# Kernel tuning notes

Hardware: AMD Instinct MI355X
Metric: run time of the kernel (lower is better)

The kernel has to match this reference:

```python
import jax, jax.numpy as jnp
import numpy as np

EPS = 0.0001
N, E, DIN, H, DH, C, G = 50000, 800000, 256, 4, 64, 10, 100


def setup_inputs() -> dict:
    key = jax.random.key(0)
    ks = jax.random.split(key, 10)
    x = jax.random.normal(ks[0], (N, DIN), dtype=jnp.float32)
    src = jax.random.randint(ks[1], (E,), 0, N)
    dst = jax.random.randint(ks[2], (E,), 0, N)
    midx = jnp.stack([src, dst]).astype(jnp.int32)
    batch = jnp.sort(jax.random.randint(ks[3], (N,), 0, G)).astype(jnp.int32)
    W_feat = jax.random.normal(ks[4], (DIN, H * DH), dtype=jnp.float32) / np.sqrt(DIN)
    phi = jax.random.normal(ks[5], (H, 2 * DH, 1), dtype=jnp.float32) / np.sqrt(2 * DH)
    W1 = jax.random.normal(ks[6], (H * DH, DH), dtype=jnp.float32) / np.sqrt(H * DH)
    b1 = jnp.zeros((DH,), jnp.float32)
    W2 = jax.random.normal(ks[7], (DH, C), dtype=jnp.float32) / np.sqrt(DH)
    b2 = jnp.zeros((C,), jnp.float32)
    return {"x": x, "midx": midx, "batch": batch, "W_feat": W_feat,
            "phi": phi, "W1": W1, "b1": b1, "W2": W2, "b2": b2}


def reference(x, midx, batch, W_feat, phi, W1, b1, W2, b2):
    src, dst = midx[0], midx[1]
    # per-head node features [N, H, DH]
    h = (x @ W_feat).reshape(-1, H, DH)
    # concat-then-matmul with phi == sum of two half projections (GAT trick)
    phi_s = phi[:, :DH, 0]   # [H, DH]
    phi_d = phi[:, DH:, 0]   # [H, DH]
    a_s = jnp.einsum('nhd,hd->nh', h, phi_s)  # [N, H]
    a_d = jnp.einsum('nhd,hd->nh', h, phi_d)
    w = jax.nn.sigmoid(jax.nn.leaky_relu(a_s[src] + a_d[dst]))  # [E, H]
    msg = (h[dst] * w[:, :, None]).reshape(src.shape[0], H * DH)  # [E, H*DH]
    agg = jax.ops.segment_sum(msg, src, num_segments=x.shape[0])  # scatter_add
    # MLP head (dropout is identity in eval mode)
    z = jax.nn.leaky_relu(agg @ W1 + b1) @ W2 + b2  # [N, C]
    tmp = jnp.exp(z - jnp.max(z, axis=-1, keepdims=True)) + EPS
    preds = tmp / jnp.sum(tmp, axis=-1, keepdims=True)
    # global mean pool over graphs
    sums = jax.ops.segment_sum(preds, batch, num_segments=G)
    cnts = jax.ops.segment_sum(jnp.ones((batch.shape[0],), preds.dtype), batch, num_segments=G)
    yp = sums / cnts[:, None]
    return jnp.log(yp), preds
```

## Files before the change

### kernel.cpp

```cpp
#include <hip/hip_runtime.h>
#include <hip/hip_bf16.h>
#include <cstdint>

#define NN   50000
#define EE   800000
#define DIN_ 256
#define HD_  256
#define DH_  64
#define NH_  4
#define NC_  10
#define NG_  100
#define EPS_ 1e-4f
#define SLOPE_ 0.01f
#define AROW 40
#define CAP_ 48
#define AGGW 5120

typedef unsigned short ushortT;
typedef __attribute__((ext_vector_type(8))) short short8;
typedef __attribute__((ext_vector_type(4))) float f32x4;

__device__ __forceinline__ float leaky(float x) { return x >= 0.f ? x : SLOPE_ * x; }
__device__ __forceinline__ float sigm(float x)  { return 1.f / (1.f + __expf(-x)); }
__device__ __forceinline__ float b2f(ushortT u) { return __uint_as_float(((unsigned)u) << 16); }
__device__ __forceinline__ ushortT f2b(float f) {
    unsigned u = __float_as_uint(f);
    u += 0x7fffu + ((u >> 16) & 1u);
    return (ushortT)(u >> 16);
}

__global__ void setup_kernel(int* cursor,
                             const float* __restrict__ W, ushortT* __restrict__ wt,
                             const float* __restrict__ W1, ushortT* __restrict__ w1t,
                             const int* __restrict__ batch, int* __restrict__ gstart) {
    int i = blockIdx.x * 256 + threadIdx.x;
    if (i < NN) {
        cursor[i] = 0;
        int b = batch[i];
        int bp = (i == 0) ? -1 : batch[i - 1];
        for (int g = bp + 1; g <= b; g++) gstart[g] = i;
        if (i == NN - 1) {
            for (int g = b + 1; g <= NG_; g++) gstart[g] = NN;
        }
    }
    if (i < DIN_ * HD_) {
        int k = i >> 8, n = i & 255;
        wt[n * DIN_ + k] = f2b(W[i]);
    }
    if (i < 256 * 64) {
        int k = i >> 6, o = i & 63;
        w1t[o * 256 + k] = f2b(W1[i]);
    }
}

__global__ __launch_bounds__(256) void gemm_attn(const float* __restrict__ x,
                                                 const ushortT* __restrict__ wt,
                                                 const float* __restrict__ phi,
                                                 ushortT* __restrict__ hbf,
                                                 float* __restrict__ a_s,
                                                 float* __restrict__ a_d) {
    __shared__ ushortT A_lds[128 * AROW];
    __shared__ ushortT B_lds[128 * AROW];
    const int tid  = threadIdx.x;
    const int wave = tid >> 6, lane = tid & 63;
    const int wm = wave >> 1, wn = wave & 1;
    const int row0 = blockIdx.x * 128;
    const int col0 = blockIdx.y * 128;
    const int q = lane >> 4, l16 = lane & 15;

    f32x4 acc[4][4];
#pragma unroll
    for (int i = 0; i < 4; i++)
#pragma unroll
        for (int j = 0; j < 4; j++) acc[i][j] = (f32x4){0.f, 0.f, 0.f, 0.f};

    const int lm  = tid >> 1;
    const int lko = (tid & 1) * 16;

    for (int k0 = 0; k0 < DIN_; k0 += 32) {
        __syncthreads();
        {
            int gr = row0 + lm;
            float4 a0 = make_float4(0.f,0.f,0.f,0.f), a1 = a0, a2 = a0, a3 = a0;
            if (gr < NN) {
                const float4* xp = (const float4*)(x + (size_t)gr * DIN_ + k0 + lko);
                a0 = xp[0]; a1 = xp[1]; a2 = xp[2]; a3 = xp[3];
            }
            ushortT* ap = &A_lds[lm * AROW + lko];
            *(ushort4*)(ap + 0)  = make_ushort4(f2b(a0.x), f2b(a0.y), f2b(a0.z), f2b(a0.w));
            *(ushort4*)(ap + 4)  = make_ushort4(f2b(a1.x), f2b(a1.y), f2b(a1.z), f2b(a1.w));
            *(ushort4*)(ap + 8)  = make_ushort4(f2b(a2.x), f2b(a2.y), f2b(a2.z), f2b(a2.w));
            *(ushort4*)(ap + 12) = make_ushort4(f2b(a3.x), f2b(a3.y), f2b(a3.z), f2b(a3.w));
        }
        {
            const uint4* wp = (const uint4*)(wt + (size_t)(col0 + lm) * DIN_ + k0 + lko);
            uint4 b0 = wp[0], b1 = wp[1];
            *(uint4*)&B_lds[lm * AROW + lko + 0] = b0;
            *(uint4*)&B_lds[lm * AROW + lko + 8] = b1;
        }
        __syncthreads();

        short8 af[4], bf[4];
#pragma unroll
        for (int mi = 0; mi < 4; mi++)
            af[mi] = *(const short8*)&A_lds[(wm * 64 + mi * 16 + l16) * AROW + q * 8];
#pragma unroll
        for (int ni = 0; ni < 4; ni++)
            bf[ni] = *(const short8*)&B_lds[(wn * 64 + ni * 16 + l16) * AROW + q * 8];
#pragma unroll
        for (int mi = 0; mi < 4; mi++)
#pragma unroll
            for (int ni = 0; ni < 4; ni++)
                acc[mi][ni] = __builtin_amdgcn_mfma_f32_16x16x32_bf16(af[mi], bf[ni], acc[mi][ni], 0, 0, 0);
    }

#pragma unroll
    for (int mi = 0; mi < 4; mi++) {
        int rbase = row0 + wm * 64 + mi * 16 + q * 4;
#pragma unroll
        for (int ni = 0; ni < 4; ni++) {
            int c = col0 + wn * 64 + ni * 16 + l16;
#pragma unroll
            for (int r = 0; r < 4; r++) {
                int gr = rbase + r;
                if (gr < NN) hbf[(size_t)gr * HD_ + c] = f2b(acc[mi][ni][r]);
            }
        }
    }

    int head = blockIdx.y * 2 + wn;
    float phs[4], phd[4];
#pragma unroll
    for (int ni = 0; ni < 4; ni++) {
        phs[ni] = phi[head * 128 + ni * 16 + l16];
        phd[ni] = phi[head * 128 + 64 + ni * 16 + l16];
    }
#pragma unroll
    for (int mi = 0; mi < 4; mi++) {
#pragma unroll
        for (int r = 0; r < 4; r++) {
            float ps = acc[mi][0][r] * phs[0] + acc[mi][1][r] * phs[1]
                     + acc[mi][2][r] * phs[2] + acc[mi][3][r] * phs[3];
            float pd = acc[mi][0][r] * phd[0] + acc[mi][1][r] * phd[1]
                     + acc[mi][2][r] * phd[2] + acc[mi][3][r] * phd[3];
#pragma unroll
            for (int o = 1; o < 16; o <<= 1) {
                ps += __shfl_xor(ps, o);
                pd += __shfl_xor(pd, o);
            }
            if (l16 == 0) {
                int gr = row0 + wm * 64 + mi * 16 + q * 4 + r;
                if (gr < NN) {
                    a_s[gr * 4 + head] = ps;
                    a_d[gr * 4 + head] = pd;
                }
            }
        }
    }
}

__global__ void fill_edges(const int* __restrict__ src, const int* __restrict__ dstA,
                           int* __restrict__ cursor,
                           const float* __restrict__ a_s, const float* __restrict__ a_d,
                           uint4* __restrict__ edges) {
    int e = blockIdx.x * 256 + threadIdx.x;
    if (e >= EE) return;
    int s = src[e], d = dstA[e];
    int slot = atomicAdd(&cursor[s], 1);
    if (slot >= CAP_) return;
    float4 as4 = *(const float4*)(a_s + (size_t)s * 4);
    float4 ad4 = *(const float4*)(a_d + (size_t)d * 4);
    unsigned w01 = (unsigned)f2b(sigm(leaky(as4.x + ad4.x)))
                 | ((unsigned)f2b(sigm(leaky(as4.y + ad4.y))) << 16);
    unsigned w23 = (unsigned)f2b(sigm(leaky(as4.z + ad4.z)))
                 | ((unsigned)f2b(sigm(leaky(as4.w + ad4.w))) << 16);
    edges[(size_t)s * CAP_ + slot] = make_uint4((unsigned)d, w01, w23, 0u);
}

__global__ __launch_bounds__(256) void agg_kernel(const ushortT* __restrict__ hbf,
                                                  const int* __restrict__ cursor,
                                                  const uint4* __restrict__ edges,
                                                  ushortT* __restrict__ aggB) {
    int wid = blockIdx.x * 4 + (threadIdx.x >> 6);
    int lane = threadIdx.x & 63;
    int hsel = lane >> 4;
    int wsh = (hsel & 1) * 16;
    const ushortT* hbase = hbf + (size_t)lane * 4;

    for (int n = wid; n < NN; n += AGGW) {
        int cnt = cursor[n];
        if (cnt > CAP_) cnt = CAP_;
        int e0 = n * CAP_, e1 = e0 + cnt;
        float4 acc = make_float4(0.f, 0.f, 0.f, 0.f);

        int i = e0;
        while (i + 8 <= e1) {
            uint4 ee[8]; ushort4 hh[8]; float ww[8];
#pragma unroll
            for (int j = 0; j < 8; j++) ee[j] = edges[i + j];
#pragma unroll
            for (int j = 0; j < 8; j++) {
                unsigned pair = (hsel & 2) ? ee[j].z : ee[j].y;
                ww[j] = b2f((ushortT)((pair >> wsh) & 0xffffu));
                hh[j] = *(const ushort4*)(hbase + (size_t)ee[j].x * HD_);
            }
#pragma unroll
            for (int j = 0; j < 8; j++) {
                acc.x += b2f(hh[j].x) * ww[j];
                acc.y += b2f(hh[j].y) * ww[j];
                acc.z += b2f(hh[j].z) * ww[j];
                acc.w += b2f(hh[j].w) * ww[j];
            }
            i += 8;
        }
        while (i + 4 <= e1) {
            uint4 ee[4]; ushort4 hh[4]; float ww[4];
#pragma unroll
            for (int j = 0; j < 4; j++) ee[j] = edges[i + j];
#pragma unroll
            for (int j = 0; j < 4; j++) {
                unsigned pair = (hsel & 2) ? ee[j].z : ee[j].y;
                ww[j] = b2f((ushortT)((pair >> wsh) & 0xffffu));
                hh[j] = *(const ushort4*)(hbase + (size_t)ee[j].x * HD_);
            }
#pragma unroll
            for (int j = 0; j < 4; j++) {
                acc.x += b2f(hh[j].x) * ww[j];
                acc.y += b2f(hh[j].y) * ww[j];
                acc.z += b2f(hh[j].z) * ww[j];
                acc.w += b2f(hh[j].w) * ww[j];
            }
            i += 4;
        }
        for (; i < e1; i++) {
            uint4 e = edges[i];
            unsigned pair = (hsel & 2) ? e.z : e.y;
            float s = b2f((ushortT)((pair >> wsh) & 0xffffu));
            ushort4 hv = *(const ushort4*)(hbase + (size_t)e.x * HD_);
            acc.x += b2f(hv.x) * s; acc.y += b2f(hv.y) * s;
            acc.z += b2f(hv.z) * s; acc.w += b2f(hv.w) * s;
        }
        ushort4 o4 = make_ushort4(f2b(acc.x), f2b(acc.y), f2b(acc.z), f2b(acc.w));
        *(ushort4*)(aggB + (size_t)n * HD_ + lane * 4) = o4;
    }
}

__global__ __launch_bounds__(256) void mlp_kernel(const ushortT* __restrict__ aggB,
                                                  const ushortT* __restrict__ w1t,
                                                  const float* __restrict__ b1,
                                                  const float* __restrict__ W2,
                                                  const float* __restrict__ b2,
                                                  float* __restrict__ out) {
    __shared__ float z1t[64][65];
    const int tid = threadIdx.x;
    const int wave = tid >> 6, lane = tid & 63;
    const int q = lane >> 4, l16 = lane & 15;
    const int n0 = blockIdx.x * 64;
    const int nodeRow = n0 + wave * 16 + l16;

    f32x4 acc[4];
#pragma unroll
    for (int ni = 0; ni < 4; ni++) acc[ni] = (f32x4){0.f, 0.f, 0.f, 0.f};

    const ushortT* arow = aggB + (size_t)nodeRow * HD_ + q * 8;
#pragma unroll
    for (int k0 = 0; k0 < 256; k0 += 32) {
        short8 af = *(const short8*)(arow + k0);
#pragma unroll
        for (int ni = 0; ni < 4; ni++) {
            short8 bf = *(const short8*)(w1t + (size_t)(ni * 16 + l16) * 256 + k0 + q * 8);
            acc[ni] = __builtin_amdgcn_mfma_f32_16x16x32_bf16(af, bf, acc[ni], 0, 0, 0);
        }
    }
#pragma unroll
    for (int ni = 0; ni < 4; ni++) {
        int o = ni * 16 + l16;
        float bb = b1[o];
#pragma unroll
        for (int r = 0; r < 4; r++)
            z1t[o][wave * 16 + q * 4 + r] = leaky(acc[ni][r] + bb);
    }
    __syncthreads();

    if (tid < 64) {
        int n = n0 + tid;
        if (n < NN) {
            float zc[NC_];
#pragma unroll
            for (int c = 0; c < NC_; c++) zc[c] = b2[c];
            for (int k = 0; k < 64; k++) {
                float zv = z1t[k][tid];
#pragma unroll
                for (int c = 0; c < NC_; c++) zc[c] += zv * W2[k * NC_ + c];
            }
            float m = zc[0];
#pragma unroll
            for (int c = 1; c < NC_; c++) m = fmaxf(m, zc[c]);
            float ssum = 0.f;
#pragma unroll
            for (int c = 0; c < NC_; c++) { zc[c] = __expf(zc[c] - m) + EPS_; ssum += zc[c]; }
            float inv = 1.f / ssum;
#pragma unroll
            for (int c = 0; c < NC_; c++) out[1000 + (size_t)n * NC_ + c] = zc[c] * inv;
        }
    }
}

__global__ __launch_bounds__(256) void group_mean(const float* __restrict__ preds,
                                                  const int* __restrict__ gstart,
                                                  float* __restrict__ out) {
    __shared__ float red[16][16];
    int g = blockIdx.x;
    int t = threadIdx.x;
    int c = t & 15, chunk = t >> 4;
    int gs = gstart[g], ge = gstart[g + 1];
    float s = 0.f;
    if (c < NC_) {
        for (int n = gs + chunk; n < ge; n += 16) s += preds[(size_t)n * NC_ + c];
    }
    red[chunk][c] = s;
    __syncthreads();
    if (t < NC_) {
        float tot = 0.f;
#pragma unroll
        for (int j = 0; j < 16; j++) tot += red[j][t];
        out[g * NC_ + t] = __logf(tot / (float)(ge - gs));
    }
}

extern "C" void kernel_launch(void* const* d_in, const int* in_sizes, int n_in,
                              void* d_out, int out_size, void* d_ws, size_t ws_size,
                              hipStream_t stream) {
    const float* x      = (const float*)d_in[0];
    const int*   midx   = (const int*)d_in[1];
    const int*   batch  = (const int*)d_in[2];
    const float* W_feat = (const float*)d_in[3];
    const float* phi    = (const float*)d_in[4];
    const float* W1     = (const float*)d_in[5];
    const float* b1     = (const float*)d_in[6];
    const float* W2     = (const float*)d_in[7];
    const float* b2     = (const float*)d_in[8];
    const int* src = midx;
    const int* dst = midx + EE;
    float* out = (float*)d_out;

    char* p = (char*)d_ws;
    auto alloc = [&](size_t bytes) { void* r = (void*)p; p += (bytes + 255) & ~(size_t)255; return r; };
    ushortT* hbf      = (ushortT*)alloc((size_t)NN * HD_ * 2);
    ushortT* aggB     = (ushortT*)alloc((size_t)NN * HD_ * 2);
    uint4*   edges    = (uint4*)alloc((size_t)NN * CAP_ * 16);
    ushortT* wt       = (ushortT*)alloc((size_t)DIN_ * HD_ * 2);
    ushortT* w1t      = (ushortT*)alloc((size_t)64 * 256 * 2);
    float*   a_s      = (float*)alloc((size_t)NN * 4 * 4);
    float*   a_d      = (float*)alloc((size_t)NN * 4 * 4);
    int*     cursor   = (int*)alloc((size_t)NN * 4);
    int*     gstart   = (int*)alloc((size_t)(NG_ + 1) * 4);

    setup_kernel<<<256, 256, 0, stream>>>(cursor, W_feat, wt, W1, w1t, batch, gstart);
    gemm_attn<<<dim3((NN + 127) / 128, 2), 256, 0, stream>>>(x, wt, phi, hbf, a_s, a_d);
    fill_edges<<<(EE + 255) / 256, 256, 0, stream>>>(src, dst, cursor, a_s, a_d, edges);
    agg_kernel<<<AGGW / 4, 256, 0, stream>>>(hbf, cursor, edges, aggB);
    mlp_kernel<<<(NN + 63) / 64, 256, 0, stream>>>(aggB, w1t, b1, W2, b2, out);
    group_mean<<<NG_, 256, 0, stream>>>(out + 1000, gstart, out);
}
```

Before: 272.7 us.

## Compute all heads per GEMM block and move edge weights into aggregation

The GEMM now computes all 256 output columns (every head) per 128-row block, so each block reads its x tile once instead of twice. Edge attention weights are no longer precomputed in fill_edges. That kernel now stores only the destination index (4 bytes instead of a 16-byte record), and the aggregation kernel computes sigmoid(leaky(a_s+a_d)) on the fly. Aggregation launches one wave per node instead of a persistent grid-stride loop. The trade-offs are higher register pressure in the GEMM, which adds launch_bounds(256,1) and doubles the accumulators, and extra a_d gathers plus transcendental work inside the aggregation.

```diff
diff --git a/kernel.cpp b/kernel.cpp
--- a/kernel.cpp
+++ b/kernel.cpp
@@ -14,7 +14,6 @@
 #define SLOPE_ 0.01f
 #define AROW 40
 #define CAP_ 48
-#define AGGW 5120
 
 typedef unsigned short ushortT;
 typedef __attribute__((ext_vector_type(8))) short short8;
@@ -53,24 +52,22 @@
     }
 }
 
-__global__ __launch_bounds__(256) void gemm_attn(const float* __restrict__ x,
-                                                 const ushortT* __restrict__ wt,
-                                                 const float* __restrict__ phi,
-                                                 ushortT* __restrict__ hbf,
-                                                 float* __restrict__ a_s,
-                                                 float* __restrict__ a_d) {
+__global__ __launch_bounds__(256, 1) void gemm_attn(const float* __restrict__ x,
+                                                    const ushortT* __restrict__ wt,
+                                                    const float* __restrict__ phi,
+                                                    ushortT* __restrict__ hbf,
+                                                    float* __restrict__ a_s,
+                                                    float* __restrict__ a_d) {
     __shared__ ushortT A_lds[128 * AROW];
-    __shared__ ushortT B_lds[128 * AROW];
+    __shared__ ushortT B_lds[256 * AROW];
     const int tid  = threadIdx.x;
     const int wave = tid >> 6, lane = tid & 63;
-    const int wm = wave >> 1, wn = wave & 1;
     const int row0 = blockIdx.x * 128;
-    const int col0 = blockIdx.y * 128;
     const int q = lane >> 4, l16 = lane & 15;
 
-    f32x4 acc[4][4];
-#pragma unroll
-    for (int i = 0; i < 4; i++)
+    f32x4 acc[8][4];
+#pragma unroll
+    for (int i = 0; i < 8; i++)
 #pragma unroll
         for (int j = 0; j < 4; j++) acc[i][j] = (f32x4){0.f, 0.f, 0.f, 0.f};
 
@@ -93,33 +90,34 @@
             *(ushort4*)(ap + 12) = make_ushort4(f2b(a3.x), f2b(a3.y), f2b(a3.z), f2b(a3.w));
         }
         {
-            const uint4* wp = (const uint4*)(wt + (size_t)(col0 + lm) * DIN_ + k0 + lko);
-            uint4 b0 = wp[0], b1 = wp[1];
-            *(uint4*)&B_lds[lm * AROW + lko + 0] = b0;
-            *(uint4*)&B_lds[lm * AROW + lko + 8] = b1;
+            const uint4* wp = (const uint4*)(wt + (size_t)tid * DIN_ + k0);
+            uint4 b0 = wp[0], b1 = wp[1], b2 = wp[2], b3 = wp[3];
+            *(uint4*)&B_lds[tid * AROW + 0]  = b0;
+            *(uint4*)&B_lds[tid * AROW + 8]  = b1;
+            *(uint4*)&B_lds[tid * AROW + 16] = b2;
+            *(uint4*)&B_lds[tid * AROW + 24] = b3;
         }
         __syncthreads();
 
-        short8 af[4], bf[4];
-#pragma unroll
-        for (int mi = 0; mi < 4; mi++)
-            af[mi] = *(const short8*)&A_lds[(wm * 64 + mi * 16 + l16) * AROW + q * 8];
+        short8 bf[4];
 #pragma unroll
         for (int ni = 0; ni < 4; ni++)
-            bf[ni] = *(const short8*)&B_lds[(wn * 64 + ni * 16 + l16) * AROW + q * 8];
-#pragma unroll
-        for (int mi = 0; mi < 4; mi++)
+            bf[ni] = *(const short8*)&B_lds[(wave * 64 + ni * 16 + l16) * AROW + q * 8];
+#pragma unroll
+        for (int mi = 0; mi < 8; mi++) {
+            short8 af = *(const short8*)&A_lds[(mi * 16 + l16) * AROW + q * 8];
 #pragma unroll
             for (int ni = 0; ni < 4; ni++)
-                acc[mi][ni] = __builtin_amdgcn_mfma_f32_16x16x32_bf16(af[mi], bf[ni], acc[mi][ni], 0, 0, 0);
-    }
-
-#pragma unroll
-    for (int mi = 0; mi < 4; mi++) {
-        int rbase = row0 + wm * 64 + mi * 16 + q * 4;
+                acc[mi][ni] = __builtin_amdgcn_mfma_f32_16x16x32_bf16(af, bf[ni], acc[mi][ni], 0, 0, 0);
+        }
+    }
+
+#pragma unroll
+    for (int mi = 0; mi < 8; mi++) {
+        int rbase = row0 + mi * 16 + q * 4;
 #pragma unroll
         for (int ni = 0; ni < 4; ni++) {
-            int c = col0 + wn * 64 + ni * 16 + l16;
+            int c = wave * 64 + ni * 16 + l16;
 #pragma unroll
             for (int r = 0; r < 4; r++) {
                 int gr = rbase + r;
@@ -128,15 +126,14 @@
         }
     }
 
-    int head = blockIdx.y * 2 + wn;
     float phs[4], phd[4];
 #pragma unroll
     for (int ni = 0; ni < 4; ni++) {
-        phs[ni] = phi[head * 128 + ni * 16 + l16];
-        phd[ni] = phi[head * 128 + 64 + ni * 16 + l16];
-    }
-#pragma unroll
-    for (int mi = 0; mi < 4; mi++) {
+        phs[ni] = phi[wave * 128 + ni * 16 + l16];
+        phd[ni] = phi[wave * 128 + 64 + ni * 16 + l16];
+    }
+#pragma unroll
+    for (int mi = 0; mi < 8; mi++) {
 #pragma unroll
         for (int r = 0; r < 4; r++) {
             float ps = acc[mi][0][r] * phs[0] + acc[mi][1][r] * phs[1]
@@ -149,10 +146,10 @@
                 pd += __shfl_xor(pd, o);
             }
             if (l16 == 0) {
-                int gr = row0 + wm * 64 + mi * 16 + q * 4 + r;
+                int gr = row0 + mi * 16 + q * 4 + r;
                 if (gr < NN) {
-                    a_s[gr * 4 + head] = ps;
-                    a_d[gr * 4 + head] = pd;
+                    a_s[gr * 4 + wave] = ps;
+                    a_d[gr * 4 + wave] = pd;
                 }
             }
         }
@@ -160,89 +157,79 @@
 }
 
 __global__ void fill_edges(const int* __restrict__ src, const int* __restrict__ dstA,
-                           int* __restrict__ cursor,
-                           const float* __restrict__ a_s, const float* __restrict__ a_d,
-                           uint4* __restrict__ edges) {
+                           int* __restrict__ cursor, int* __restrict__ edge_dst) {
     int e = blockIdx.x * 256 + threadIdx.x;
     if (e >= EE) return;
-    int s = src[e], d = dstA[e];
+    int s = src[e];
     int slot = atomicAdd(&cursor[s], 1);
     if (slot >= CAP_) return;
-    float4 as4 = *(const float4*)(a_s + (size_t)s * 4);
-    float4 ad4 = *(const float4*)(a_d + (size_t)d * 4);
-    unsigned w01 = (unsigned)f2b(sigm(leaky(as4.x + ad4.x)))
-                 | ((unsigned)f2b(sigm(leaky(as4.y + ad4.y))) << 16);
-    unsigned w23 = (unsigned)f2b(sigm(leaky(as4.z + ad4.z)))
-                 | ((unsigned)f2b(sigm(leaky(as4.w + ad4.w))) << 16);
-    edges[(size_t)s * CAP_ + slot] = make_uint4((unsigned)d, w01, w23, 0u);
+    edge_dst[s * CAP_ + slot] = dstA[e];
 }
 
 __global__ __launch_bounds__(256) void agg_kernel(const ushortT* __restrict__ hbf,
                                                   const int* __restrict__ cursor,
-                                                  const uint4* __restrict__ edges,
+                                                  const int* __restrict__ edge_dst,
+                                                  const float* __restrict__ a_s,
+                                                  const float* __restrict__ a_d,
                                                   ushortT* __restrict__ aggB) {
-    int wid = blockIdx.x * 4 + (threadIdx.x >> 6);
-    int lane = threadIdx.x & 63;
+    int wv = threadIdx.x >> 6, lane = threadIdx.x & 63;
+    int n = blockIdx.x * 4 + wv;
     int hsel = lane >> 4;
-    int wsh = (hsel & 1) * 16;
+    int cnt = cursor[n];
+    if (cnt > CAP_) cnt = CAP_;
+    int e0 = n * CAP_, e1 = e0 + cnt;
+    float as_h = a_s[n * 4 + hsel];
+    float4 acc = make_float4(0.f, 0.f, 0.f, 0.f);
     const ushortT* hbase = hbf + (size_t)lane * 4;
 
-    for (int n = wid; n < NN; n += AGGW) {
-        int cnt = cursor[n];
-        if (cnt > CAP_) cnt = CAP_;
-        int e0 = n * CAP_, e1 = e0 + cnt;
-        float4 acc = make_float4(0.f, 0.f, 0.f, 0.f);
-
-        int i = e0;
-        while (i + 8 <= e1) {
-            uint4 ee[8]; ushort4 hh[8]; float ww[8];
-#pragma unroll
-            for (int j = 0; j < 8; j++) ee[j] = edges[i + j];
-#pragma unroll
-            for (int j = 0; j < 8; j++) {
-                unsigned pair = (hsel & 2) ? ee[j].z : ee[j].y;
-                ww[j] = b2f((ushortT)((pair >> wsh) & 0xffffu));
-                hh[j] = *(const ushort4*)(hbase + (size_t)ee[j].x * HD_);
-            }
-#pragma unroll
-            for (int j = 0; j < 8; j++) {
-                acc.x += b2f(hh[j].x) * ww[j];
-                acc.y += b2f(hh[j].y) * ww[j];
-                acc.z += b2f(hh[j].z) * ww[j];
-                acc.w += b2f(hh[j].w) * ww[j];
-            }
-            i += 8;
-        }
-        while (i + 4 <= e1) {
-            uint4 ee[4]; ushort4 hh[4]; float ww[4];
-#pragma unroll
-            for (int j = 0; j < 4; j++) ee[j] = edges[i + j];
-#pragma unroll
-            for (int j = 0; j < 4; j++) {
-                unsigned pair = (hsel & 2) ? ee[j].z : ee[j].y;
-                ww[j] = b2f((ushortT)((pair >> wsh) & 0xffffu));
-                hh[j] = *(const ushort4*)(hbase + (size_t)ee[j].x * HD_);
-            }
-#pragma unroll
-            for (int j = 0; j < 4; j++) {
-                acc.x += b2f(hh[j].x) * ww[j];
-                acc.y += b2f(hh[j].y) * ww[j];
-                acc.z += b2f(hh[j].z) * ww[j];
-                acc.w += b2f(hh[j].w) * ww[j];
-            }
-            i += 4;
-        }
-        for (; i < e1; i++) {
-            uint4 e = edges[i];
-            unsigned pair = (hsel & 2) ? e.z : e.y;
-            float s = b2f((ushortT)((pair >> wsh) & 0xffffu));
-            ushort4 hv = *(const ushort4*)(hbase + (size_t)e.x * HD_);
-            acc.x += b2f(hv.x) * s; acc.y += b2f(hv.y) * s;
-            acc.z += b2f(hv.z) * s; acc.w += b2f(hv.w) * s;
-        }
-        ushort4 o4 = make_ushort4(f2b(acc.x), f2b(acc.y), f2b(acc.z), f2b(acc.w));
-        *(ushort4*)(aggB + (size_t)n * HD_ + lane * 4) = o4;
-    }
+    int i = e0;
+    while (i + 8 <= e1) {
+        int dd[8]; float ad[8]; ushort4 hh[8];
+#pragma unroll
+        for (int j = 0; j < 8; j++) dd[j] = edge_dst[i + j];
+#pragma unroll
+        for (int j = 0; j < 8; j++) {
+            ad[j] = a_d[dd[j] * 4 + hsel];
+            hh[j] = *(const ushort4*)(hbase + (size_t)dd[j] * HD_);
+        }
+#pragma unroll
+        for (int j = 0; j < 8; j++) {
+            float w = sigm(leaky(as_h + ad[j]));
+            acc.x += b2f(hh[j].x) * w;
+            acc.y += b2f(hh[j].y) * w;
+            acc.z += b2f(hh[j].z) * w;
+            acc.w += b2f(hh[j].w) * w;
+        }
+        i += 8;
+    }
+    while (i + 4 <= e1) {
+        int dd[4]; float ad[4]; ushort4 hh[4];
+#pragma unroll
+        for (int j = 0; j < 4; j++) dd[j] = edge_dst[i + j];
+#pragma unroll
+        for (int j = 0; j < 4; j++) {
+            ad[j] = a_d[dd[j] * 4 + hsel];
+            hh[j] = *(const ushort4*)(hbase + (size_t)dd[j] * HD_);
+        }
+#pragma unroll
+        for (int j = 0; j < 4; j++) {
+            float w = sigm(leaky(as_h + ad[j]));
+            acc.x += b2f(hh[j].x) * w;
+            acc.y += b2f(hh[j].y) * w;
+            acc.z += b2f(hh[j].z) * w;
+            acc.w += b2f(hh[j].w) * w;
+        }
+        i += 4;
+    }
+    for (; i < e1; i++) {
+        int d = edge_dst[i];
+        float w = sigm(leaky(as_h + a_d[d * 4 + hsel]));
+        ushort4 hv = *(const ushort4*)(hbase + (size_t)d * HD_);
+        acc.x += b2f(hv.x) * w; acc.y += b2f(hv.y) * w;
+        acc.z += b2f(hv.z) * w; acc.w += b2f(hv.w) * w;
+    }
+    ushort4 o4 = make_ushort4(f2b(acc.x), f2b(acc.y), f2b(acc.z), f2b(acc.w));
+    *(ushort4*)(aggB + (size_t)n * HD_ + lane * 4) = o4;
 }
 
 __global__ __launch_bounds__(256) void mlp_kernel(const ushortT* __restrict__ aggB,
@@ -348,7 +335,7 @@
     auto alloc = [&](size_t bytes) { void* r = (void*)p; p += (bytes + 255) & ~(size_t)255; return r; };
     ushortT* hbf      = (ushortT*)alloc((size_t)NN * HD_ * 2);
     ushortT* aggB     = (ushortT*)alloc((size_t)NN * HD_ * 2);
-    uint4*   edges    = (uint4*)alloc((size_t)NN * CAP_ * 16);
+    int*     edge_dst = (int*)alloc((size_t)NN * CAP_ * 4);
     ushortT* wt       = (ushortT*)alloc((size_t)DIN_ * HD_ * 2);
     ushortT* w1t      = (ushortT*)alloc((size_t)64 * 256 * 2);
     float*   a_s      = (float*)alloc((size_t)NN * 4 * 4);
@@ -357,9 +344,9 @@
     int*     gstart   = (int*)alloc((size_t)(NG_ + 1) * 4);
 
     setup_kernel<<<256, 256, 0, stream>>>(cursor, W_feat, wt, W1, w1t, batch, gstart);
-    gemm_attn<<<dim3((NN + 127) / 128, 2), 256, 0, stream>>>(x, wt, phi, hbf, a_s, a_d);
-    fill_edges<<<(EE + 255) / 256, 256, 0, stream>>>(src, dst, cursor, a_s, a_d, edges);
-    agg_kernel<<<AGGW / 4, 256, 0, stream>>>(hbf, cursor, edges, aggB);
+    gemm_attn<<<(NN + 127) / 128, 256, 0, stream>>>(x, wt, phi, hbf, a_s, a_d);
+    fill_edges<<<(EE + 255) / 256, 256, 0, stream>>>(src, dst, cursor, edge_dst);
+    agg_kernel<<<NN / 4, 256, 0, stream>>>(hbf, cursor, edge_dst, a_s, a_d, aggB);
     mlp_kernel<<<(NN + 63) / 64, 256, 0, stream>>>(aggB, w1t, b1, W2, b2, out);
     group_mean<<<NG_, 256, 0, stream>>>(out + 1000, gstart, out);
 }
```

Result: slower. 284.8 us (+4.4%).
